# Performance work log

Hardware: AMD Instinct MI355X
Metric: run time of the kernel (lower is better)

The kernel has to match this reference:

```python
import jax, jax.numpy as jnp
import numpy as np

B, S, E, H, F = 4, 2048, 1024, 16, 4096
D = E // H
EPS = 1e-5

def _layernorm(x, g, b):
    mu = jnp.mean(x, axis=-1, keepdims=True)
    var = jnp.mean((x - mu) ** 2, axis=-1, keepdims=True)
    return (x - mu) * jax.lax.rsqrt(var + EPS) * g + b

def setup_inputs() -> dict:
    key = jax.random.key(0)
    ks = jax.random.split(key, 16)
    s_e = 1.0 / np.sqrt(E)
    s_f = 1.0 / np.sqrt(F)
    return {
        "x": jax.random.normal(ks[0], (B, S, E), jnp.float32),
        "qw": jax.random.uniform(ks[1], (E, E), jnp.float32, -s_e, s_e),
        "qb": jax.random.uniform(ks[2], (E,), jnp.float32, -s_e, s_e),
        "kw": jax.random.uniform(ks[3], (E, E), jnp.float32, -s_e, s_e),
        "kb": jax.random.uniform(ks[4], (E,), jnp.float32, -s_e, s_e),
        "vw": jax.random.uniform(ks[5], (E, E), jnp.float32, -s_e, s_e),
        "vb": jax.random.uniform(ks[6], (E,), jnp.float32, -s_e, s_e),
        "ow": jax.random.uniform(ks[7], (E, E), jnp.float32, -s_e, s_e),
        "ob": jax.random.uniform(ks[8], (E,), jnp.float32, -s_e, s_e),
        "ln1_g": jnp.ones((E,), jnp.float32),
        "ln1_b": jnp.zeros((E,), jnp.float32),
        "w1": jax.random.uniform(ks[9], (E, F), jnp.float32, -s_e, s_e),
        "b1": jax.random.uniform(ks[10], (F,), jnp.float32, -s_e, s_e),
        "w2": jax.random.uniform(ks[11], (F, E), jnp.float32, -s_f, s_f),
        "b2": jax.random.uniform(ks[12], (E,), jnp.float32, -s_f, s_f),
        "ln2_g": jnp.ones((E,), jnp.float32),
        "ln2_b": jnp.zeros((E,), jnp.float32),
    }

def reference(x, qw, qb, kw, kb, vw, vb, ow, ob, ln1_g, ln1_b, w1, b1, w2, b2, ln2_g, ln2_b):
    # --- multi-head self-attention ---
    q = (x @ qw + qb).reshape(B, S, H, D).transpose(0, 2, 1, 3)  # [B,H,S,D]
    k = (x @ kw + kb).reshape(B, S, H, D).transpose(0, 2, 1, 3)
    v = (x @ vw + vb).reshape(B, S, H, D).transpose(0, 2, 1, 3)
    scores = jnp.einsum('bhqd,bhkd->bhqk', q, k) / jnp.sqrt(jnp.float32(D))
    attn = jax.nn.softmax(scores, axis=-1)
    attended = jnp.einsum('bhqk,bhkd->bhqd', attn, v)
    attended = attended.transpose(0, 2, 1, 3).reshape(B, S, E)
    attn_out = attended @ ow + ob
    # --- residual + norm1 ---
    h = _layernorm(x + attn_out, ln1_g, ln1_b)
    # --- feed forward ---
    ff = jax.nn.relu(h @ w1 + b1) @ w2 + b2
    # --- residual + norm2 ---
    return _layernorm(h + ff, ln2_g, ln2_b)
```

## Files before the change

### kernel.cpp

```cpp
#include <hip/hip_runtime.h>
#include <hip/hip_bf16.h>

typedef unsigned short u16;
typedef unsigned int u32;
typedef __attribute__((ext_vector_type(8))) short bf16x8;
typedef __attribute__((ext_vector_type(4))) float f32x4;
typedef __attribute__((ext_vector_type(16))) float f32x16;
typedef __attribute__((ext_vector_type(8))) unsigned short u16x8;
typedef __attribute__((ext_vector_type(4))) unsigned short u16x4;

#define B_ 4
#define S_ 2048
#define E_ 1024
#define H_ 16
#define D_ 64
#define F_ 4096
#define M_ 8192

__device__ __forceinline__ float bf2f(u16 u) {
    union { unsigned int i; float f; } v; v.i = ((unsigned int)u) << 16; return v.f;
}
__device__ __forceinline__ u16 f2bf(float f) {
    union { float f; unsigned int i; } v; v.f = f;
    unsigned int r = v.i + 0x7FFFu + ((v.i >> 16) & 1u);
    return (u16)(r >> 16);
}

__global__ __launch_bounds__(256) void cast_f32_bf16(const float* __restrict__ in,
                                                     u16* __restrict__ out) {
    const int i = blockIdx.x * 256 + threadIdx.x;
    const f32x4* p = (const f32x4*)in + (size_t)i * 2;
    f32x4 a = p[0], b = p[1];
    u16x8 o;
    o[0] = f2bf(a[0]); o[1] = f2bf(a[1]); o[2] = f2bf(a[2]); o[3] = f2bf(a[3]);
    o[4] = f2bf(b[0]); o[5] = f2bf(b[1]); o[6] = f2bf(b[2]); o[7] = f2bf(b[3]);
    *((u16x8*)out + i) = o;
}

__global__ __launch_bounds__(256) void transpose_cast(const float* __restrict__ w,
                                                      u16* __restrict__ wT,
                                                      int R, int C) {
    __shared__ float tile[32][33];
    const int tx = threadIdx.x & 31, ty = threadIdx.x >> 5;
    const int c0 = blockIdx.x * 32, r0 = blockIdx.y * 32;
#pragma unroll
    for (int i = 0; i < 4; ++i)
        tile[ty + i * 8][tx] = w[(size_t)(r0 + ty + i * 8) * C + c0 + tx];
    __syncthreads();
#pragma unroll
    for (int i = 0; i < 4; ++i)
        wT[(size_t)(c0 + ty + i * 8) * R + r0 + tx] = f2bf(tile[tx][ty + i * 8]);
}

__global__ __launch_bounds__(256) void concat_bias(const float* __restrict__ qb,
                                                   const float* __restrict__ kb,
                                                   const float* __restrict__ vb,
                                                   float* __restrict__ dst) {
    const int i = blockIdx.x * 256 + threadIdx.x;
    float v = (i < 1024) ? qb[i] : ((i < 2048) ? kb[i - 1024] : vb[i - 2048]);
    dst[i] = v;
}

__global__ __launch_bounds__(256) void transpose_kv(const u16* __restrict__ qkv,
                                                    u16* __restrict__ vt,
                                                    u16* __restrict__ kc) {
    __shared__ u16 t2[64 * 66];
    const int s0 = blockIdx.x * 64;
    const int bh = blockIdx.y;
    const int b = bh >> 4, h = bh & 15;
    const size_t ksec = ((size_t)b * S_) * 3072 + 1024 + (size_t)h * 64;
    const size_t vsec = ((size_t)b * S_) * 3072 + 2048 + (size_t)h * 64;
    const int t = threadIdx.x;
    const int sr = t >> 3, dc = (t & 7) * 8;
#pragma unroll
    for (int p = 0; p < 2; ++p) {
        const int s = sr + p * 32;
        u16x8 kv = *(const u16x8*)(qkv + ksec + (size_t)(s0 + s) * 3072 + dc);
        *(u16x8*)(kc + ((size_t)bh * S_ + s0 + s) * 64 + dc) = kv;
        u16x8 v = *(const u16x8*)(qkv + vsec + (size_t)(s0 + s) * 3072 + dc);
#pragma unroll
        for (int e = 0; e < 8; ++e) t2[(dc + e) * 66 + s] = v[e];
    }
    __syncthreads();
    const int dr = t >> 3, sc2 = (t & 7) * 8;
#pragma unroll
    for (int p = 0; p < 2; ++p) {
        const int d = dr + p * 32;
        u16x8 o;
#pragma unroll
        for (int e = 0; e < 8; ++e) o[e] = t2[d * 66 + sc2 + e];
        *(u16x8*)(vt + (((size_t)bh * 32 + blockIdx.x) * 64 + d) * 64 + sc2) = o;
    }
}

#define STAGEA(dst, kt) { \
    _Pragma("unroll") for (int h_ = 0; h_ < 2; ++h_) \
    _Pragma("unroll") for (int j_ = 0; j_ < 2; ++j_) \
        __builtin_amdgcn_global_load_lds( \
            (const __attribute__((address_space(1))) void*)(Ag + (size_t)(h_ * 128 + j_ * 64) * Kb + (size_t)(kt) * 128), \
            (__attribute__((address_space(3))) void*)((char*)(dst) + h_ * 16384 + j_ * 8192 + ldst), 16, 0, 0); }

#define STAGEB(dst, kt) { \
    _Pragma("unroll") for (int h_ = 0; h_ < BN / 128; ++h_) \
    _Pragma("unroll") for (int j_ = 0; j_ < 2; ++j_) \
        __builtin_amdgcn_global_load_lds( \
            (const __attribute__((address_space(1))) void*)(Bg + (size_t)(h_ * 128 + j_ * 64) * Kb + (size_t)(kt) * 128), \
            (__attribute__((address_space(3))) void*)((char*)(dst) + h_ * 16384 + j_ * 8192 + ldst), 16, 0, 0); }

#define LOADA(buf, mg) { \
    _Pragma("unroll") for (int m_ = 0; m_ < 4; ++m_) \
    _Pragma("unroll") for (int kh_ = 0; kh_ < 2; ++kh_) \
        af[m_][kh_] = *(const bf16x8*)((const char*)(buf) + wm * 16384 + ((mg) * 64 + m_ * 16 + lr) * 128 + ((kh_ * 64 + lg * 16) ^ swr)); }

#define LOADB(buf, ng) { \
    _Pragma("unroll") for (int n_ = 0; n_ < NR / 2; ++n_) \
    _Pragma("unroll") for (int kh_ = 0; kh_ < 2; ++kh_) { \
        const int brow_ = wn * (BN / 4) + ((ng) * (NR / 2) + n_) * 16 + lr; \
        bfr[(ng) * (NR / 2) + n_][kh_] = *(const bf16x8*)((const char*)(buf) + (brow_ >> 7) * 16384 + (brow_ & 127) * 128 + ((kh_ * 64 + lg * 16) ^ swr)); } }

#define MFMAQ(mg, ng) { \
    __builtin_amdgcn_s_setprio(1); \
    _Pragma("unroll") for (int m_ = 0; m_ < 4; ++m_) \
    _Pragma("unroll") for (int n_ = 0; n_ < NR / 2; ++n_) \
    _Pragma("unroll") for (int kh_ = 0; kh_ < 2; ++kh_) \
        acc[(mg) * 4 + m_][(ng) * (NR / 2) + n_] = __builtin_amdgcn_mfma_f32_16x16x32_bf16( \
            af[m_][kh_], bfr[(ng) * (NR / 2) + n_][kh_], acc[(mg) * 4 + m_][(ng) * (NR / 2) + n_], 0, 0, 0); \
    __builtin_amdgcn_s_setprio(0); }

#define VMWAIT0 { asm volatile("s_waitcnt vmcnt(0)" ::: "memory"); __builtin_amdgcn_sched_barrier(0); }

template<int NR>
__global__ __launch_bounds__(512, 2) void gemm8p(const u16* __restrict__ A,
                                                 const u16* __restrict__ Bt,
                                                 const float* __restrict__ bias,
                                                 u16* __restrict__ C,
                                                 int N, int K, int relu) {
    constexpr int BN = NR * 64;
    constexpr int ASZ = 16384;
    constexpr int BSZ = BN * 64;
    __shared__ __align__(16) u16 lds[2 * (ASZ + BSZ)];
    u16* const As0 = lds;
    u16* const Bs0 = lds + ASZ;
    u16* const As1 = lds + ASZ + BSZ;
    u16* const Bs1 = lds + 2 * ASZ + BSZ;

    const int tid = threadIdx.x;
    const int wid = tid >> 6, lane = tid & 63;
    const int wm = wid >> 2, wn = wid & 3;
    const int lr = lane & 15, lg = lane >> 4;
    const int swr = (lr & 7) << 4;
    const int mbase = blockIdx.y * 256, nbase = blockIdx.x * BN;

    const int r8 = tid >> 3;
    const int swc = ((tid & 7) * 16) ^ ((r8 & 7) << 4);
    const size_t Kb = (size_t)K * 2;
    const char* Ag = (const char*)A + (size_t)(mbase + r8) * Kb + swc;
    const char* Bg = (const char*)Bt + (size_t)(nbase + r8) * Kb + swc;
    const int ldst = tid * 16;

    f32x4 acc[8][NR];
    const f32x4 z = {0.f, 0.f, 0.f, 0.f};
#pragma unroll
    for (int m = 0; m < 8; ++m)
#pragma unroll
        for (int n = 0; n < NR; ++n) acc[m][n] = z;

    bf16x8 af[4][2], bfr[NR][2];

    STAGEA(As0, 0);
    STAGEB(Bs0, 0);
    VMWAIT0;
    __builtin_amdgcn_s_barrier();

    const int niter = K >> 7;
    for (int i = 0; i < niter; ++i) {
        const int kt1 = 2 * i + 1, kt2 = 2 * i + 2;
        LOADA(As0, 0); LOADB(Bs0, 0);
        STAGEA(As1, kt1);
        MFMAQ(0, 0);
        __builtin_amdgcn_s_barrier();
        LOADB(Bs0, 1);
        STAGEB(Bs1, kt1);
        MFMAQ(0, 1);
        __builtin_amdgcn_s_barrier();
        LOADA(As0, 1);
        MFMAQ(1, 0);
        __builtin_amdgcn_s_barrier();
        MFMAQ(1, 1);
        VMWAIT0;
        __builtin_amdgcn_s_barrier();
        LOADA(As1, 0); LOADB(Bs1, 0);
        if (i + 1 < niter) STAGEA(As0, kt2);
        MFMAQ(0, 0);
        __builtin_amdgcn_s_barrier();
        LOADB(Bs1, 1);
        if (i + 1 < niter) STAGEB(Bs0, kt2);
        MFMAQ(0, 1);
        __builtin_amdgcn_s_barrier();
        LOADA(As1, 1);
        MFMAQ(1, 0);
        __builtin_amdgcn_s_barrier();
        MFMAQ(1, 1);
        VMWAIT0;
        __builtin_amdgcn_s_barrier();
    }

#pragma unroll
    for (int m = 0; m < 8; ++m) {
        const int row0 = mbase + wm * 128 + m * 16 + lg * 4;
#pragma unroll
        for (int n = 0; n < NR; ++n) {
            const int col = nbase + wn * (BN / 4) + n * 16 + lr;
            const float bz = bias[col];
#pragma unroll
            for (int r = 0; r < 4; ++r) {
                float v = acc[m][n][r] + bz;
                if (relu) v = fmaxf(v, 0.f);
                C[(size_t)(row0 + r) * N + col] = f2bf(v);
            }
        }
    }
}

__device__ __forceinline__ u32 cvtpk_bf16(float lo, float hi2) {
    u32 r;
    asm("v_cvt_pk_bf16_f32 %0, %1, %2" : "=v"(r) : "v"(lo), "v"(hi2));
    return r;
}
__global__ __launch_bounds__(256) void attn_flash6(const u16* __restrict__ qkv,
                                                   const u16* __restrict__ kcg,
                                                   const u16* __restrict__ vtg,
                                                   u16* __restrict__ att) {
    __shared__ __align__(16) u16 Kt[2][64 * 64];
    __shared__ __align__(16) u16 Vt[2][64 * 64];
    const int tid = threadIdx.x, wid = tid >> 6;
    const int lane = tid & 63, l31 = lane & 31, hi = lane >> 5;
    const int bh = blockIdx.y, b = bh >> 4, h = bh & 15;
    const size_t tok0 = (size_t)b * S_;
    const int q0 = blockIdx.x * 128 + wid * 32;

    bf16x8 qf[4];
    {
        const u16* qp = qkv + (tok0 + q0 + l31) * 3072 + h * 64 + hi * 8;
#pragma unroll
        for (int dc = 0; dc < 4; ++dc) qf[dc] = *(const bf16x8*)(qp + dc * 16);
    }

    const int srow = tid >> 3;
    const int scolb = ((tid & 7) * 16) ^ ((srow & 7) << 4);
    const u16* kbase = kcg + ((size_t)bh * S_ + srow) * 64 + (scolb >> 1);
    const u16* vbase = vtg + (size_t)bh * 32 * 4096 + srow * 64 + (scolb >> 1);
    const int ldst = tid * 16;

    f32x16 acco0, acco1;
#pragma unroll
    for (int r = 0; r < 16; ++r) { acco0[r] = 0.f; acco1[r] = 0.f; }
    float m_reg = -1e30f, l_run = 0.f;

    __builtin_amdgcn_global_load_lds((const __attribute__((address_space(1))) void*)kbase,
        (__attribute__((address_space(3))) void*)((char*)Kt[0] + ldst), 16, 0, 0);
    __builtin_amdgcn_global_load_lds((const __attribute__((address_space(1))) void*)(kbase + 32 * 64),
        (__attribute__((address_space(3))) void*)((char*)Kt[0] + 4096 + ldst), 16, 0, 0);
    __builtin_amdgcn_global_load_lds((const __attribute__((address_space(1))) void*)vbase,
        (__attribute__((address_space(3))) void*)((char*)Vt[0] + ldst), 16, 0, 0);
    __builtin_amdgcn_global_load_lds((const __attribute__((address_space(1))) void*)(vbase + 32 * 64),
        (__attribute__((address_space(3))) void*)((char*)Vt[0] + 4096 + ldst), 16, 0, 0);
    __syncthreads();

    const float CSC = 0.125f * 1.44269504088896341f;
    const int hb4 = hi * 16;

    for (int kt = 0; kt < 32; ++kt) {
        const int cur = kt & 1;
        if (kt + 1 < 32) {
            const size_t adv = (size_t)(kt + 1) * 4096;
            __builtin_amdgcn_global_load_lds((const __attribute__((address_space(1))) void*)(kbase + adv),
                (__attribute__((address_space(3))) void*)((char*)Kt[cur ^ 1] + ldst), 16, 0, 0);
            __builtin_amdgcn_global_load_lds((const __attribute__((address_space(1))) void*)(kbase + adv + 32 * 64),
                (__attribute__((address_space(3))) void*)((char*)Kt[cur ^ 1] + 4096 + ldst), 16, 0, 0);
            __builtin_amdgcn_global_load_lds((const __attribute__((address_space(1))) void*)(vbase + adv),
                (__attribute__((address_space(3))) void*)((char*)Vt[cur ^ 1] + ldst), 16, 0, 0);
            __builtin_amdgcn_global_load_lds((const __attribute__((address_space(1))) void*)(vbase + adv + 32 * 64),
                (__attribute__((address_space(3))) void*)((char*)Vt[cur ^ 1] + 4096 + ldst), 16, 0, 0);
        }

        f32x16 p0, p1;
#pragma unroll
        for (int r = 0; r < 16; ++r) { p0[r] = 0.f; p1[r] = 0.f; }
        __builtin_amdgcn_s_setprio(1);
#pragma unroll
        for (int dc = 0; dc < 4; ++dc) {
            const int row0 = l31, row1 = 32 + l31;
            const bf16x8 kf0 = *(const bf16x8*)((const char*)Kt[cur] + row0 * 128 + ((dc * 32 + hi * 16) ^ ((row0 & 7) << 4)));
            const bf16x8 kf1 = *(const bf16x8*)((const char*)Kt[cur] + row1 * 128 + ((dc * 32 + hi * 16) ^ ((row1 & 7) << 4)));
            p0 = __builtin_amdgcn_mfma_f32_32x32x16_bf16(kf0, qf[dc], p0, 0, 0, 0);
            p1 = __builtin_amdgcn_mfma_f32_32x32x16_bf16(kf1, qf[dc], p1, 0, 0, 0);
        }
        __builtin_amdgcn_s_setprio(0);

        float mx = p0[0];
#pragma unroll
        for (int r = 1; r < 16; ++r) mx = fmaxf(mx, p0[r]);
#pragma unroll
        for (int r = 0; r < 16; ++r) mx = fmaxf(mx, p1[r]);
        float sa = mx, sb = mx;
        asm volatile("v_permlane32_swap_b32 %0, %1" : "+v"(sa), "+v"(sb));
        const float fullm = fmaxf(sa, sb) * CSC;

        if (!__all(fullm - m_reg <= 8.0f)) {
            const float mnew = fmaxf(m_reg, fullm);
            const float alf = exp2f(m_reg - mnew);
            l_run *= alf;
            m_reg = mnew;
            const int au = __float_as_int(alf);
#pragma unroll
            for (int r = 0; r < 16; ++r) {
                const int addr = ((r & 3) + 8 * (r >> 2)) * 4 + hb4;
                const float ar = __int_as_float(__builtin_amdgcn_ds_bpermute(addr, au));
                acco0[r] *= ar;
                acco1[r] *= ar;
            }
        }

        float pe0[16], pe1[16];
        float ls = 0.f;
#pragma unroll
        for (int r = 0; r < 16; ++r) {
            pe0[r] = exp2f(__builtin_fmaf(p0[r], CSC, -m_reg));
            pe1[r] = exp2f(__builtin_fmaf(p1[r], CSC, -m_reg));
            ls += pe0[r] + pe1[r];
        }
        l_run += ls;

        union { u32 u[4]; bf16x8 v; } pa0, pa1, pa2, pa3;
        {
            u32 a, bswap, c, d;
            a = cvtpk_bf16(pe0[0], pe0[1]);  bswap = cvtpk_bf16(pe0[4], pe0[5]);
            asm volatile("v_permlane32_swap_b32 %0, %1" : "+v"(a), "+v"(bswap));
            c = cvtpk_bf16(pe0[2], pe0[3]);  d = cvtpk_bf16(pe0[6], pe0[7]);
            asm volatile("v_permlane32_swap_b32 %0, %1" : "+v"(c), "+v"(d));
            pa0.u[0] = a; pa0.u[1] = c; pa0.u[2] = bswap; pa0.u[3] = d;
            a = cvtpk_bf16(pe0[8], pe0[9]);  bswap = cvtpk_bf16(pe0[12], pe0[13]);
            asm volatile("v_permlane32_swap_b32 %0, %1" : "+v"(a), "+v"(bswap));
            c = cvtpk_bf16(pe0[10], pe0[11]); d = cvtpk_bf16(pe0[14], pe0[15]);
            asm volatile("v_permlane32_swap_b32 %0, %1" : "+v"(c), "+v"(d));
            pa1.u[0] = a; pa1.u[1] = c; pa1.u[2] = bswap; pa1.u[3] = d;
            a = cvtpk_bf16(pe1[0], pe1[1]);  bswap = cvtpk_bf16(pe1[4], pe1[5]);
            asm volatile("v_permlane32_swap_b32 %0, %1" : "+v"(a), "+v"(bswap));
            c = cvtpk_bf16(pe1[2], pe1[3]);  d = cvtpk_bf16(pe1[6], pe1[7]);
            asm volatile("v_permlane32_swap_b32 %0, %1" : "+v"(c), "+v"(d));
            pa2.u[0] = a; pa2.u[1] = c; pa2.u[2] = bswap; pa2.u[3] = d;
            a = cvtpk_bf16(pe1[8], pe1[9]);  bswap = cvtpk_bf16(pe1[12], pe1[13]);
            asm volatile("v_permlane32_swap_b32 %0, %1" : "+v"(a), "+v"(bswap));
            c = cvtpk_bf16(pe1[10], pe1[11]); d = cvtpk_bf16(pe1[14], pe1[15]);
            asm volatile("v_permlane32_swap_b32 %0, %1" : "+v"(c), "+v"(d));
            pa3.u[0] = a; pa3.u[1] = c; pa3.u[2] = bswap; pa3.u[3] = d;
        }

        __builtin_amdgcn_s_setprio(1);
#pragma unroll
        for (int dblk = 0; dblk < 2; ++dblk) {
            const int row = dblk * 32 + l31;
            const int sw = (row & 7) << 4;
            const char* vrow = (const char*)Vt[cur] + row * 128;
            const bf16x8 v0 = *(const bf16x8*)(vrow + ((0 * 32 + hi * 16) ^ sw));
            const bf16x8 v1 = *(const bf16x8*)(vrow + ((1 * 32 + hi * 16) ^ sw));
            const bf16x8 v2 = *(const bf16x8*)(vrow + ((2 * 32 + hi * 16) ^ sw));
            const bf16x8 v3 = *(const bf16x8*)(vrow + ((3 * 32 + hi * 16) ^ sw));
            if (dblk == 0) {
                acco0 = __builtin_amdgcn_mfma_f32_32x32x16_bf16(pa0.v, v0, acco0, 0, 0, 0);
                acco0 = __builtin_amdgcn_mfma_f32_32x32x16_bf16(pa1.v, v1, acco0, 0, 0, 0);
                acco0 = __builtin_amdgcn_mfma_f32_32x32x16_bf16(pa2.v, v2, acco0, 0, 0, 0);
                acco0 = __builtin_amdgcn_mfma_f32_32x32x16_bf16(pa3.v, v3, acco0, 0, 0, 0);
            } else {
                acco1 = __builtin_amdgcn_mfma_f32_32x32x16_bf16(pa0.v, v0, acco1, 0, 0, 0);
                acco1 = __builtin_amdgcn_mfma_f32_32x32x16_bf16(pa1.v, v1, acco1, 0, 0, 0);
                acco1 = __builtin_amdgcn_mfma_f32_32x32x16_bf16(pa2.v, v2, acco1, 0, 0, 0);
                acco1 = __builtin_amdgcn_mfma_f32_32x32x16_bf16(pa3.v, v3, acco1, 0, 0, 0);
            }
        }
        __builtin_amdgcn_s_setprio(0);

        __syncthreads();
    }

    float la = l_run, lb = l_run;
    asm volatile("v_permlane32_swap_b32 %0, %1" : "+v"(la), "+v"(lb));
    const float linv = 1.0f / (la + lb);
    const int li = __float_as_int(linv);
#pragma unroll
    for (int r = 0; r < 16; ++r) {
        const int addr = ((r & 3) + 8 * (r >> 2)) * 4 + hb4;
        const float lr = __int_as_float(__builtin_amdgcn_ds_bpermute(addr, li));
        const int qrow = (r & 3) + 8 * (r >> 2) + 4 * hi;
        u16* orow = att + (tok0 + q0 + qrow) * E_ + h * 64 + l31;
        orow[0]  = f2bf(acco0[r] * lr);
        orow[32] = f2bf(acco1[r] * lr);
    }
}

__global__ __launch_bounds__(256) void ln_fused(const float* __restrict__ xr,
                                                const u16* __restrict__ yb,
                                                const float* __restrict__ g,
                                                const float* __restrict__ bb,
                                                float* __restrict__ ho,
                                                u16* __restrict__ hb) {
    const int wid = threadIdx.x >> 6, lane = threadIdx.x & 63;
    const int row = blockIdx.x * 4 + wid;
    const float* xp = xr + (size_t)row * E_;
    const u16* yp = yb + (size_t)row * E_;

    f32x4 t[4];
    float sum = 0.f, ss = 0.f;
#pragma unroll
    for (int j = 0; j < 4; ++j) {
        const int idx = j * 256 + lane * 4;
        const f32x4 xv = *(const f32x4*)(xp + idx);
        const u16x4 yv = *(const u16x4*)(yp + idx);
        f32x4 tv;
#pragma unroll
        for (int e = 0; e < 4; ++e) tv[e] = xv[e] + bf2f(yv[e]);
        t[j] = tv;
        sum += tv[0] + tv[1] + tv[2] + tv[3];
        ss += tv[0] * tv[0] + tv[1] * tv[1] + tv[2] * tv[2] + tv[3] * tv[3];
    }
#pragma unroll
    for (int off = 1; off < 64; off <<= 1) {
        sum += __shfl_xor(sum, off);
        ss += __shfl_xor(ss, off);
    }
    const float mu = sum * (1.f / 1024.f);
    const float var = ss * (1.f / 1024.f) - mu * mu;
    const float rstd = rsqrtf(var + 1e-5f);
#pragma unroll
    for (int j = 0; j < 4; ++j) {
        const int idx = j * 256 + lane * 4;
        const f32x4 gv = *(const f32x4*)(g + idx);
        const f32x4 bv = *(const f32x4*)(bb + idx);
        f32x4 ov;
#pragma unroll
        for (int e = 0; e < 4; ++e) ov[e] = (t[j][e] - mu) * rstd * gv[e] + bv[e];
        *(f32x4*)(ho + (size_t)row * E_ + idx) = ov;
        if (hb) {
            u16x4 o4;
#pragma unroll
            for (int e = 0; e < 4; ++e) o4[e] = f2bf(ov[e]);
            *(u16x4*)(hb + (size_t)row * E_ + idx) = o4;
        }
    }
}

extern "C" void kernel_launch(void* const* d_in, const int* in_sizes, int n_in,
                              void* d_out, int out_size, void* d_ws, size_t ws_size,
                              hipStream_t stream) {
    const float* x    = (const float*)d_in[0];
    const float* qw   = (const float*)d_in[1];
    const float* qb   = (const float*)d_in[2];
    const float* kw   = (const float*)d_in[3];
    const float* kb   = (const float*)d_in[4];
    const float* vw   = (const float*)d_in[5];
    const float* vb   = (const float*)d_in[6];
    const float* ow   = (const float*)d_in[7];
    const float* ob   = (const float*)d_in[8];
    const float* ln1g = (const float*)d_in[9];
    const float* ln1b = (const float*)d_in[10];
    const float* w1   = (const float*)d_in[11];
    const float* b1   = (const float*)d_in[12];
    const float* w2   = (const float*)d_in[13];
    const float* b2   = (const float*)d_in[14];
    const float* ln2g = (const float*)d_in[15];
    const float* ln2b = (const float*)d_in[16];

    if (ws_size < 192950272ull) return;

    char* ws = (char*)d_ws;
    u16*  wqkvT = (u16*)(ws + 0);
    u16*  woT   = (u16*)(ws + 6291456);
    u16*  w1T   = (u16*)(ws + 8388608);
    u16*  w2T   = (u16*)(ws + 16777216);
    float* bqkv = (float*)(ws + 25165824);
    u16*  xb    = (u16*)(ws + 25178112);
    u16*  attb  = xb;
    u16*  qkvb  = (u16*)(ws + 41955328);
    u16*  aob   = qkvb;
    u16*  vtg   = (u16*)(ws + 58732544);
    u16*  hbb   = (u16*)(ws + 58732544);
    u16*  ff2b  = (u16*)(ws + 75509760);
    float* hf   = (float*)(ws + 92286976);
    u16*  ff1b  = (u16*)(ws + 125841408);
    u16*  kcg   = (u16*)(ws + 125841408);

    cast_f32_bf16<<<dim3(4096), dim3(256), 0, stream>>>(x, xb);
    transpose_cast<<<dim3(32, 32), dim3(256), 0, stream>>>(qw, wqkvT, 1024, 1024);
    transpose_cast<<<dim3(32, 32), dim3(256), 0, stream>>>(kw, wqkvT + 1024 * 1024, 1024, 1024);
    transpose_cast<<<dim3(32, 32), dim3(256), 0, stream>>>(vw, wqkvT + 2048 * 1024, 1024, 1024);
    transpose_cast<<<dim3(32, 32), dim3(256), 0, stream>>>(ow, woT, 1024, 1024);
    transpose_cast<<<dim3(128, 32), dim3(256), 0, stream>>>(w1, w1T, 1024, 4096);
    transpose_cast<<<dim3(32, 128), dim3(256), 0, stream>>>(w2, w2T, 4096, 1024);
    concat_bias<<<dim3(12), dim3(256), 0, stream>>>(qb, kb, vb, bqkv);

    gemm8p<4><<<dim3(12, 32), dim3(512), 0, stream>>>(xb, wqkvT, bqkv, qkvb, 3072, 1024, 0);
    transpose_kv<<<dim3(32, 64), dim3(256), 0, stream>>>(qkvb, vtg, kcg);
    attn_flash6<<<dim3(16, 64), dim3(256), 0, stream>>>(qkvb, kcg, vtg, attb);
    gemm8p<2><<<dim3(8, 32), dim3(512), 0, stream>>>(attb, woT, ob, aob, 1024, 1024, 0);
    ln_fused<<<dim3(2048), dim3(256), 0, stream>>>(x, aob, ln1g, ln1b, hf, hbb);
    gemm8p<4><<<dim3(16, 32), dim3(512), 0, stream>>>(hbb, w1T, b1, ff1b, 4096, 1024, 1);
    gemm8p<2><<<dim3(8, 32), dim3(512), 0, stream>>>(ff1b, w2T, b2, ff2b, 1024, 4096, 0);
    ln_fused<<<dim3(2048), dim3(256), 0, stream>>>(hf, ff2b, ln2g, ln2b, (float*)d_out, (u16*)nullptr);
}
```

Baseline: 469.3 us.

## Merge prep kernels, remap workgroups for XCD locality, compute softmax denominator via MFMA

All weight and input cast/transpose kernels and the bias concat are merged into one prep launch. GEMM and attention workgroup IDs are remapped so neighbouring tiles land on the same XCD and share L2. Attention now reads K directly from the strided QKV buffer instead of a packed copy, which removes the K copy from the transpose kernel. The softmax row sum is accumulated with an extra MFMA against a ones vector rather than with scalar adds and cross-lane shuffles. This trims launch overhead, copy traffic and VALU work, at the cost of strided K loads and four extra MFMAs per tile.

After: 417.9 us. -11.0%, faster.

```diff
diff --git a/kernel.cpp b/kernel.cpp
--- a/kernel.cpp
+++ b/kernel.cpp
@@ -26,57 +26,76 @@
     return (u16)(r >> 16);
 }
 
-__global__ __launch_bounds__(256) void cast_f32_bf16(const float* __restrict__ in,
-                                                     u16* __restrict__ out) {
-    const int i = blockIdx.x * 256 + threadIdx.x;
-    const f32x4* p = (const f32x4*)in + (size_t)i * 2;
-    f32x4 a = p[0], b = p[1];
-    u16x8 o;
-    o[0] = f2bf(a[0]); o[1] = f2bf(a[1]); o[2] = f2bf(a[2]); o[3] = f2bf(a[3]);
-    o[4] = f2bf(b[0]); o[5] = f2bf(b[1]); o[6] = f2bf(b[2]); o[7] = f2bf(b[3]);
-    *((u16x8*)out + i) = o;
-}
-
-__global__ __launch_bounds__(256) void transpose_cast(const float* __restrict__ w,
-                                                      u16* __restrict__ wT,
-                                                      int R, int C) {
+__global__ __launch_bounds__(256) void prep_all(const float* __restrict__ x, u16* __restrict__ xb,
+                                                const float* __restrict__ qw, const float* __restrict__ kw,
+                                                const float* __restrict__ vw, const float* __restrict__ ow,
+                                                const float* __restrict__ w1, const float* __restrict__ w2,
+                                                u16* __restrict__ wqkvT, u16* __restrict__ woT,
+                                                u16* __restrict__ w1T, u16* __restrict__ w2T,
+                                                const float* __restrict__ qb, const float* __restrict__ kb,
+                                                const float* __restrict__ vb, float* __restrict__ bqkv) {
     __shared__ float tile[32][33];
-    const int tx = threadIdx.x & 31, ty = threadIdx.x >> 5;
-    const int c0 = blockIdx.x * 32, r0 = blockIdx.y * 32;
+    const int bid = blockIdx.x;
+    const int tid = threadIdx.x;
+    if (bid < 4096) {
+        const int i = bid * 256 + tid;
+        const f32x4* p = (const f32x4*)x + (size_t)i * 2;
+        f32x4 a = p[0], b = p[1];
+        u16x8 o;
+        o[0] = f2bf(a[0]); o[1] = f2bf(a[1]); o[2] = f2bf(a[2]); o[3] = f2bf(a[3]);
+        o[4] = f2bf(b[0]); o[5] = f2bf(b[1]); o[6] = f2bf(b[2]); o[7] = f2bf(b[3]);
+        *((u16x8*)xb + i) = o;
+        return;
+    }
+    if (bid >= 16384) {
+        const int i = (bid - 16384) * 256 + tid;
+        float v = (i < 1024) ? qb[i] : ((i < 2048) ? kb[i - 1024] : vb[i - 2048]);
+        bqkv[i] = v;
+        return;
+    }
+    const float* src; u16* dst; int R, C, bx, by;
+    if (bid < 8192) {
+        const int t = (bid - 4096) >> 10, lb = (bid - 4096) & 1023;
+        R = 1024; C = 1024;
+        bx = lb & 31; by = lb >> 5;
+        if (t == 0)      { src = qw; dst = wqkvT; }
+        else if (t == 1) { src = kw; dst = wqkvT + 1024 * 1024; }
+        else if (t == 2) { src = vw; dst = wqkvT + 2048 * 1024; }
+        else             { src = ow; dst = woT; }
+    } else if (bid < 12288) {
+        const int lb = bid - 8192;
+        R = 1024; C = 4096;
+        bx = lb & 127; by = lb >> 7;
+        src = w1; dst = w1T;
+    } else {
+        const int lb = bid - 12288;
+        R = 4096; C = 1024;
+        bx = lb & 31; by = lb >> 5;
+        src = w2; dst = w2T;
+    }
+    const int tx = tid & 31, ty = tid >> 5;
+    const int c0 = bx * 32, r0 = by * 32;
 #pragma unroll
     for (int i = 0; i < 4; ++i)
-        tile[ty + i * 8][tx] = w[(size_t)(r0 + ty + i * 8) * C + c0 + tx];
+        tile[ty + i * 8][tx] = src[(size_t)(r0 + ty + i * 8) * C + c0 + tx];
     __syncthreads();
 #pragma unroll
     for (int i = 0; i < 4; ++i)
-        wT[(size_t)(c0 + ty + i * 8) * R + r0 + tx] = f2bf(tile[tx][ty + i * 8]);
-}
-
-__global__ __launch_bounds__(256) void concat_bias(const float* __restrict__ qb,
-                                                   const float* __restrict__ kb,
-                                                   const float* __restrict__ vb,
-                                                   float* __restrict__ dst) {
-    const int i = blockIdx.x * 256 + threadIdx.x;
-    float v = (i < 1024) ? qb[i] : ((i < 2048) ? kb[i - 1024] : vb[i - 2048]);
-    dst[i] = v;
-}
-
-__global__ __launch_bounds__(256) void transpose_kv(const u16* __restrict__ qkv,
-                                                    u16* __restrict__ vt,
-                                                    u16* __restrict__ kc) {
+        dst[(size_t)(c0 + ty + i * 8) * R + r0 + tx] = f2bf(tile[tx][ty + i * 8]);
+}
+
+__global__ __launch_bounds__(256) void transpose_v(const u16* __restrict__ qkv,
+                                                   u16* __restrict__ vt) {
     __shared__ u16 t2[64 * 66];
     const int s0 = blockIdx.x * 64;
     const int bh = blockIdx.y;
     const int b = bh >> 4, h = bh & 15;
-    const size_t ksec = ((size_t)b * S_) * 3072 + 1024 + (size_t)h * 64;
     const size_t vsec = ((size_t)b * S_) * 3072 + 2048 + (size_t)h * 64;
     const int t = threadIdx.x;
     const int sr = t >> 3, dc = (t & 7) * 8;
 #pragma unroll
     for (int p = 0; p < 2; ++p) {
         const int s = sr + p * 32;
-        u16x8 kv = *(const u16x8*)(qkv + ksec + (size_t)(s0 + s) * 3072 + dc);
-        *(u16x8*)(kc + ((size_t)bh * S_ + s0 + s) * 64 + dc) = kv;
         u16x8 v = *(const u16x8*)(qkv + vsec + (size_t)(s0 + s) * 3072 + dc);
 #pragma unroll
         for (int e = 0; e < 8; ++e) t2[(dc + e) * 66 + s] = v[e];
@@ -149,7 +168,13 @@
     const int wm = wid >> 2, wn = wid & 3;
     const int lr = lane & 15, lg = lane >> 4;
     const int swr = (lr & 7) << 4;
-    const int mbase = blockIdx.y * 256, nbase = blockIdx.x * BN;
+
+    int lin = blockIdx.y * gridDim.x + blockIdx.x;
+    const int nwg = gridDim.x * gridDim.y;
+    const int cpx = nwg >> 3;
+    lin = (lin & 7) * cpx + (lin >> 3);
+    const int bxn = lin % gridDim.x, byn = lin / gridDim.x;
+    const int mbase = byn * 256, nbase = bxn * BN;
 
     const int r8 = tid >> 3;
     const int swc = ((tid & 7) * 16) ^ ((r8 & 7) << 4);
@@ -227,17 +252,19 @@
     asm("v_cvt_pk_bf16_f32 %0, %1, %2" : "=v"(r) : "v"(lo), "v"(hi2));
     return r;
 }
-__global__ __launch_bounds__(256) void attn_flash6(const u16* __restrict__ qkv,
-                                                   const u16* __restrict__ kcg,
+__global__ __launch_bounds__(256) void attn_flash7(const u16* __restrict__ qkv,
                                                    const u16* __restrict__ vtg,
                                                    u16* __restrict__ att) {
     __shared__ __align__(16) u16 Kt[2][64 * 64];
     __shared__ __align__(16) u16 Vt[2][64 * 64];
     const int tid = threadIdx.x, wid = tid >> 6;
     const int lane = tid & 63, l31 = lane & 31, hi = lane >> 5;
-    const int bh = blockIdx.y, b = bh >> 4, h = bh & 15;
+    int lin = blockIdx.y * 16 + blockIdx.x;
+    lin = (lin & 7) * 128 + (lin >> 3);
+    const int bh = lin >> 4, qt = lin & 15;
+    const int b = bh >> 4, h = bh & 15;
     const size_t tok0 = (size_t)b * S_;
-    const int q0 = blockIdx.x * 128 + wid * 32;
+    const int q0 = qt * 128 + wid * 32;
 
     bf16x8 qf[4];
     {
@@ -248,18 +275,21 @@
 
     const int srow = tid >> 3;
     const int scolb = ((tid & 7) * 16) ^ ((srow & 7) << 4);
-    const u16* kbase = kcg + ((size_t)bh * S_ + srow) * 64 + (scolb >> 1);
+    const u16* kbase = qkv + (tok0 + srow) * 3072 + 1024 + h * 64 + (scolb >> 1);
     const u16* vbase = vtg + (size_t)bh * 32 * 4096 + srow * 64 + (scolb >> 1);
     const int ldst = tid * 16;
 
-    f32x16 acco0, acco1;
-#pragma unroll
-    for (int r = 0; r < 16; ++r) { acco0[r] = 0.f; acco1[r] = 0.f; }
-    float m_reg = -1e30f, l_run = 0.f;
+    f32x16 acco0, acco1, lacc;
+#pragma unroll
+    for (int r = 0; r < 16; ++r) { acco0[r] = 0.f; acco1[r] = 0.f; lacc[r] = 0.f; }
+    float m_reg = -1e30f;
+    const f32x16 z16 = {0.f,0.f,0.f,0.f,0.f,0.f,0.f,0.f,0.f,0.f,0.f,0.f,0.f,0.f,0.f,0.f};
+    const short oneb = (short)0x3F80;
+    const bf16x8 onesv = {oneb, oneb, oneb, oneb, oneb, oneb, oneb, oneb};
 
     __builtin_amdgcn_global_load_lds((const __attribute__((address_space(1))) void*)kbase,
         (__attribute__((address_space(3))) void*)((char*)Kt[0] + ldst), 16, 0, 0);
-    __builtin_amdgcn_global_load_lds((const __attribute__((address_space(1))) void*)(kbase + 32 * 64),
+    __builtin_amdgcn_global_load_lds((const __attribute__((address_space(1))) void*)(kbase + 32 * 3072),
         (__attribute__((address_space(3))) void*)((char*)Kt[0] + 4096 + ldst), 16, 0, 0);
     __builtin_amdgcn_global_load_lds((const __attribute__((address_space(1))) void*)vbase,
         (__attribute__((address_space(3))) void*)((char*)Vt[0] + ldst), 16, 0, 0);
@@ -273,36 +303,35 @@
     for (int kt = 0; kt < 32; ++kt) {
         const int cur = kt & 1;
         if (kt + 1 < 32) {
-            const size_t adv = (size_t)(kt + 1) * 4096;
-            __builtin_amdgcn_global_load_lds((const __attribute__((address_space(1))) void*)(kbase + adv),
+            const size_t advk = (size_t)(kt + 1) * 64 * 3072;
+            const size_t advv = (size_t)(kt + 1) * 4096;
+            __builtin_amdgcn_global_load_lds((const __attribute__((address_space(1))) void*)(kbase + advk),
                 (__attribute__((address_space(3))) void*)((char*)Kt[cur ^ 1] + ldst), 16, 0, 0);
-            __builtin_amdgcn_global_load_lds((const __attribute__((address_space(1))) void*)(kbase + adv + 32 * 64),
+            __builtin_amdgcn_global_load_lds((const __attribute__((address_space(1))) void*)(kbase + advk + 32 * 3072),
                 (__attribute__((address_space(3))) void*)((char*)Kt[cur ^ 1] + 4096 + ldst), 16, 0, 0);
-            __builtin_amdgcn_global_load_lds((const __attribute__((address_space(1))) void*)(vbase + adv),
+            __builtin_amdgcn_global_load_lds((const __attribute__((address_space(1))) void*)(vbase + advv),
                 (__attribute__((address_space(3))) void*)((char*)Vt[cur ^ 1] + ldst), 16, 0, 0);
-            __builtin_amdgcn_global_load_lds((const __attribute__((address_space(1))) void*)(vbase + adv + 32 * 64),
+            __builtin_amdgcn_global_load_lds((const __attribute__((address_space(1))) void*)(vbase + advv + 32 * 64),
                 (__attribute__((address_space(3))) void*)((char*)Vt[cur ^ 1] + 4096 + ldst), 16, 0, 0);
         }
 
         f32x16 p0, p1;
-#pragma unroll
-        for (int r = 0; r < 16; ++r) { p0[r] = 0.f; p1[r] = 0.f; }
         __builtin_amdgcn_s_setprio(1);
 #pragma unroll
         for (int dc = 0; dc < 4; ++dc) {
             const int row0 = l31, row1 = 32 + l31;
             const bf16x8 kf0 = *(const bf16x8*)((const char*)Kt[cur] + row0 * 128 + ((dc * 32 + hi * 16) ^ ((row0 & 7) << 4)));
             const bf16x8 kf1 = *(const bf16x8*)((const char*)Kt[cur] + row1 * 128 + ((dc * 32 + hi * 16) ^ ((row1 & 7) << 4)));
-            p0 = __builtin_amdgcn_mfma_f32_32x32x16_bf16(kf0, qf[dc], p0, 0, 0, 0);
-            p1 = __builtin_amdgcn_mfma_f32_32x32x16_bf16(kf1, qf[dc], p1, 0, 0, 0);
+            p0 = __builtin_amdgcn_mfma_f32_32x32x16_bf16(kf0, qf[dc], dc == 0 ? z16 : p0, 0, 0, 0);
+            p1 = __builtin_amdgcn_mfma_f32_32x32x16_bf16(kf1, qf[dc], dc == 0 ? z16 : p1, 0, 0, 0);
         }
         __builtin_amdgcn_s_setprio(0);
 
-        float mx = p0[0];
-#pragma unroll
-        for (int r = 1; r < 16; ++r) mx = fmaxf(mx, p0[r]);
-#pragma unroll
-        for (int r = 0; r < 16; ++r) mx = fmaxf(mx, p1[r]);
+        float mx = fmaxf(p0[0], p0[1]);
+#pragma unroll
+        for (int r = 2; r < 16; r += 2) mx = fmaxf(fmaxf(mx, p0[r]), p0[r + 1]);
+#pragma unroll
+        for (int r = 0; r < 16; r += 2) mx = fmaxf(fmaxf(mx, p1[r]), p1[r + 1]);
         float sa = mx, sb = mx;
         asm volatile("v_permlane32_swap_b32 %0, %1" : "+v"(sa), "+v"(sb));
         const float fullm = fmaxf(sa, sb) * CSC;
@@ -310,7 +339,6 @@
         if (!__all(fullm - m_reg <= 8.0f)) {
             const float mnew = fmaxf(m_reg, fullm);
             const float alf = exp2f(m_reg - mnew);
-            l_run *= alf;
             m_reg = mnew;
             const int au = __float_as_int(alf);
 #pragma unroll
@@ -319,18 +347,16 @@
                 const float ar = __int_as_float(__builtin_amdgcn_ds_bpermute(addr, au));
                 acco0[r] *= ar;
                 acco1[r] *= ar;
+                lacc[r] *= ar;
             }
         }
 
         float pe0[16], pe1[16];
-        float ls = 0.f;
 #pragma unroll
         for (int r = 0; r < 16; ++r) {
             pe0[r] = exp2f(__builtin_fmaf(p0[r], CSC, -m_reg));
             pe1[r] = exp2f(__builtin_fmaf(p1[r], CSC, -m_reg));
-            ls += pe0[r] + pe1[r];
-        }
-        l_run += ls;
+        }
 
         union { u32 u[4]; bf16x8 v; } pa0, pa1, pa2, pa3;
         {
@@ -358,6 +384,10 @@
         }
 
         __builtin_amdgcn_s_setprio(1);
+        lacc = __builtin_amdgcn_mfma_f32_32x32x16_bf16(pa0.v, onesv, lacc, 0, 0, 0);
+        lacc = __builtin_amdgcn_mfma_f32_32x32x16_bf16(pa1.v, onesv, lacc, 0, 0, 0);
+        lacc = __builtin_amdgcn_mfma_f32_32x32x16_bf16(pa2.v, onesv, lacc, 0, 0, 0);
+        lacc = __builtin_amdgcn_mfma_f32_32x32x16_bf16(pa3.v, onesv, lacc, 0, 0, 0);
 #pragma unroll
         for (int dblk = 0; dblk < 2; ++dblk) {
             const int row = dblk * 32 + l31;
@@ -384,14 +414,9 @@
         __syncthreads();
     }
 
-    float la = l_run, lb = l_run;
-    asm volatile("v_permlane32_swap_b32 %0, %1" : "+v"(la), "+v"(lb));
-    const float linv = 1.0f / (la + lb);
-    const int li = __float_as_int(linv);
 #pragma unroll
     for (int r = 0; r < 16; ++r) {
-        const int addr = ((r & 3) + 8 * (r >> 2)) * 4 + hb4;
-        const float lr = __int_as_float(__builtin_amdgcn_ds_bpermute(addr, li));
+        const float lr = 1.0f / lacc[r];
         const int qrow = (r & 3) + 8 * (r >> 2) + 4 * hi;
         u16* orow = att + (tok0 + q0 + qrow) * E_ + h * 64 + l31;
         orow[0]  = f2bf(acco0[r] * lr);
@@ -488,20 +513,12 @@
     u16*  ff2b  = (u16*)(ws + 75509760);
     float* hf   = (float*)(ws + 92286976);
     u16*  ff1b  = (u16*)(ws + 125841408);
-    u16*  kcg   = (u16*)(ws + 125841408);
-
-    cast_f32_bf16<<<dim3(4096), dim3(256), 0, stream>>>(x, xb);
-    transpose_cast<<<dim3(32, 32), dim3(256), 0, stream>>>(qw, wqkvT, 1024, 1024);
-    transpose_cast<<<dim3(32, 32), dim3(256), 0, stream>>>(kw, wqkvT + 1024 * 1024, 1024, 1024);
-    transpose_cast<<<dim3(32, 32), dim3(256), 0, stream>>>(vw, wqkvT + 2048 * 1024, 1024, 1024);
-    transpose_cast<<<dim3(32, 32), dim3(256), 0, stream>>>(ow, woT, 1024, 1024);
-    transpose_cast<<<dim3(128, 32), dim3(256), 0, stream>>>(w1, w1T, 1024, 4096);
-    transpose_cast<<<dim3(32, 128), dim3(256), 0, stream>>>(w2, w2T, 4096, 1024);
-    concat_bias<<<dim3(12), dim3(256), 0, stream>>>(qb, kb, vb, bqkv);
-
+
+    prep_all<<<dim3(16396), dim3(256), 0, stream>>>(x, xb, qw, kw, vw, ow, w1, w2,
+                                                    wqkvT, woT, w1T, w2T, qb, kb, vb, bqkv);
     gemm8p<4><<<dim3(12, 32), dim3(512), 0, stream>>>(xb, wqkvT, bqkv, qkvb, 3072, 1024, 0);
-    transpose_kv<<<dim3(32, 64), dim3(256), 0, stream>>>(qkvb, vtg, kcg);
-    attn_flash6<<<dim3(16, 64), dim3(256), 0, stream>>>(qkvb, kcg, vtg, attb);
+    transpose_v<<<dim3(32, 64), dim3(256), 0, stream>>>(qkvb, vtg);
+    attn_flash7<<<dim3(16, 64), dim3(256), 0, stream>>>(qkvb, vtg, attb);
     gemm8p<2><<<dim3(8, 32), dim3(512), 0, stream>>>(attb, woT, ob, aob, 1024, 1024, 0);
     ln_fused<<<dim3(2048), dim3(256), 0, stream>>>(x, aob, ln1g, ln1b, hf, hbb);
     gemm8p<4><<<dim3(16, 32), dim3(512), 0, stream>>>(hbb, w1T, b1, ff1b, 4096, 1024, 1);
```
